# Kernel optimization log

Hardware: AMD Instinct MI355X
Metric: run time of the kernel (lower is better)

The kernel has to match this reference:

```python
import jax, jax.numpy as jnp
import numpy as np

OUT = 7        # RoIPool output_size
STRIDE = 16    # feature map stride (forward does cat_rois[:,1:] *= 1/16)


def setup_inputs() -> dict:
    key = jax.random.key(0)
    k1, k2, k3 = jax.random.split(key, 3)
    B, C, H, W, N = 2, 256, 50, 50, 128
    features = jax.random.normal(k1, (B, C, H, W), jnp.float32)
    im = jax.random.randint(k2, (N,), 0, B).astype(jnp.float32)
    # image-space coords in [0, 16*(H-1)] so rounded feature coords stay in-bounds
    coords = jax.random.uniform(k3, (N, 4), jnp.float32, 0.0, float(STRIDE * (H - 1)))
    x1 = jnp.minimum(coords[:, 0], coords[:, 2])
    x2 = jnp.maximum(coords[:, 0], coords[:, 2])
    y1 = jnp.minimum(coords[:, 1], coords[:, 3])
    y2 = jnp.maximum(coords[:, 1], coords[:, 3])
    cat_rois = jnp.stack([im, x1, y1, x2, y2], axis=1)
    return {"features": features, "cat_rois": cat_rois}


def _roi_pool(features, cat_rois):
    # cat_rois[:,1:] *= 1/16 ; round ; cast to int (as in the torch module)
    rois = cat_rois.at[:, 1:].multiply(1.0 / STRIDE)
    rois = jnp.round(rois).astype(jnp.int32)
    im = rois[:, 0]
    x1, y1, x2, y2 = rois[:, 1], rois[:, 2], rois[:, 3], rois[:, 4]
    h = y2 - y1 + 1  # slice y1:y2+1 -> height
    w = x2 - x1 + 1
    H, W = features.shape[2], features.shape[3]

    i = jnp.arange(OUT)
    # AdaptiveMaxPool2d bin boundaries: start=floor(i*h/OUT), end=ceil((i+1)*h/OUT)
    ys = (i[None, :] * h[:, None]) // OUT + y1[:, None]                 # [N,OUT]
    ye = ((i[None, :] + 1) * h[:, None] + OUT - 1) // OUT + y1[:, None]
    xs = (i[None, :] * w[:, None]) // OUT + x1[:, None]
    xe = ((i[None, :] + 1) * w[:, None] + OUT - 1) // OUT + x1[:, None]

    r = jnp.arange(H)
    c = jnp.arange(W)
    row_mask = (r[None, None, :] >= ys[:, :, None]) & (r[None, None, :] < ye[:, :, None])  # [N,OUT,H]
    col_mask = (c[None, None, :] >= xs[:, :, None]) & (c[None, None, :] < xe[:, :, None])  # [N,OUT,W]

    feat = features[im]  # gather per-roi image: [N,C,H,W]
    neg = jnp.finfo(features.dtype).min
    # row pooling: small fixed loop over OUT bins; select fuses into reduce-max
    rp = jnp.stack(
        [jnp.max(jnp.where(row_mask[:, i, :][:, None, :, None], feat, neg), axis=2)
         for i in range(OUT)], axis=2)  # [N,C,OUT,W]
    out = jnp.stack(
        [jnp.max(jnp.where(col_mask[:, j, :][:, None, None, :], rp, neg), axis=3)
         for j in range(OUT)], axis=3)  # [N,C,OUT,OUT]
    return out


def reference(features, cat_rois):
    return _roi_pool(features, cat_rois)
```

## Files before the change

kernel.cpp:

```cpp
#include <hip/hip_runtime.h>
#include <float.h>

#define OUTP 7
#define NCH 256
#define FH 50
#define FW 50
#define LDS_W 65

__global__ __launch_bounds__(256) void roi_pool_v5(
    const float* __restrict__ features,
    const float* __restrict__ cat_rois,
    float* __restrict__ out)
{
    __shared__ float rowmax[4][OUTP][LDS_W];

    const int lane = threadIdx.x & 63;
    const int quad = threadIdx.x >> 6;
    const int n    = blockIdx.x >> 6;
    const int c    = ((blockIdx.x & 63) << 2) + quad;

    const float* r5 = cat_rois + n * 5;
    const int im = __builtin_amdgcn_readfirstlane((int)rintf(r5[0]));
    const int x1 = __builtin_amdgcn_readfirstlane((int)rintf(r5[1] * 0.0625f));
    const int y1 = __builtin_amdgcn_readfirstlane((int)rintf(r5[2] * 0.0625f));
    const int x2 = __builtin_amdgcn_readfirstlane((int)rintf(r5[3] * 0.0625f));
    const int y2 = __builtin_amdgcn_readfirstlane((int)rintf(r5[4] * 0.0625f));

    const int h = y2 - y1 + 1;
    const int w = x2 - x1 + 1;

    const float* base = features + ((size_t)(im * NCH + c)) * (FH * FW)
                                 + y1 * FW + x1;

    float rm[OUTP];
    #pragma unroll
    for (int i = 0; i < OUTP; ++i) rm[i] = -FLT_MAX;

    if (lane < w) {
        if (h <= 21) {
            #pragma unroll
            for (int i = 0; i < OUTP; ++i) {
                const int ys  = i * h / OUTP;
                const int ye1 = ((i + 1) * h + OUTP - 1) / OUTP - 1;
                float v0 = base[ys * FW + lane];
                float v1 = base[min(ys + 1, ye1) * FW + lane];
                float v2 = base[min(ys + 2, ye1) * FW + lane];
                float v3 = base[min(ys + 3, ye1) * FW + lane];
                rm[i] = fmaxf(fmaxf(v0, v1), fmaxf(v2, v3));
            }
        } else {
            #pragma unroll
            for (int i = 0; i < OUTP; ++i) {
                const int ys  = i * h / OUTP;
                const int ye1 = ((i + 1) * h + OUTP - 1) / OUTP - 1;
                float v[8];
                #pragma unroll
                for (int k = 0; k < 8; ++k)
                    v[k] = base[min(ys + k, ye1) * FW + lane];
                float m01 = fmaxf(v[0], v[1]), m23 = fmaxf(v[2], v[3]);
                float m45 = fmaxf(v[4], v[5]), m67 = fmaxf(v[6], v[7]);
                rm[i] = fmaxf(fmaxf(m01, m23), fmaxf(m45, m67));
            }
        }
    }

    #pragma unroll
    for (int i = 0; i < OUTP; ++i)
        rowmax[quad][i][lane] = rm[i];

    __syncthreads();

    if (lane < OUTP * OUTP) {
        const int i  = lane / OUTP;
        const int j  = lane % OUTP;
        const int xs = j * w / OUTP;
        const int xe = ((j + 1) * w + OUTP - 1) / OUTP;

        float m = -FLT_MAX;
        for (int x = xs; x < xe; ++x)
            m = fmaxf(m, rowmax[quad][i][x]);

        out[(((size_t)n * NCH + c) * OUTP + i) * OUTP + j] = m;
    }
}

extern "C" void kernel_launch(void* const* d_in, const int* in_sizes, int n_in,
                              void* d_out, int out_size, void* d_ws, size_t ws_size,
                              hipStream_t stream) {
    const float* features = (const float*)d_in[0];
    const float* cat_rois = (const float*)d_in[1];
    float* out = (float*)d_out;

    const int N = in_sizes[1] / 5;
    dim3 grid(N * (NCH / 4));
    roi_pool_v5<<<grid, 256, 0, stream>>>(features, cat_rois, out);
}
```

Measured before the change: 73.34 us.

## Pack multiple channels per wavefront by ROI width, 16 channels per block

Each wavefront now handles 4 channels instead of 1. Narrow ROIs (w<=16 or w<=32) pack 4 or 2 channels into the 64 lanes at once so fewer lanes sit idle; wide ROIs loop over the channels. The grid shrinks fourfold and the block-wide __syncthreads is replaced with per-wave LDS waitcnt fences, since each wave only touches its own LDS slice. In exchange there are fewer blocks and more serial work per wave, and correctness now depends on the in-wave LDS ordering being right.

New measurement: 70.80 us. 1.04x faster.

```diff
diff --git a/kernel.cpp b/kernel.cpp
--- a/kernel.cpp
+++ b/kernel.cpp
@@ -5,19 +5,78 @@
 #define NCH 256
 #define FH 50
 #define FW 50
-#define LDS_W 65
+#define LDS_P 65
+#define CH_PER_BLOCK 16
 
-__global__ __launch_bounds__(256) void roi_pool_v5(
+
+template<int KMAX>
+__device__ __forceinline__ void row_phase(const float* __restrict__ lb, int h,
+                                          bool active, float (&rm)[OUTP])
+{
+    #pragma unroll
+    for (int i = 0; i < OUTP; ++i) rm[i] = -FLT_MAX;
+    if (active) {
+        #pragma unroll
+        for (int i = 0; i < OUTP; ++i) {
+            const int ys  = i * h / OUTP;
+            const int ye1 = ((i + 1) * h + OUTP - 1) / OUTP - 1;
+            float v[KMAX];
+            #pragma unroll
+            for (int k = 0; k < KMAX; ++k)
+                v[k] = lb[min(ys + k, ye1) * FW];
+            #pragma unroll
+            for (int s = KMAX / 2; s > 0; s >>= 1)
+                #pragma unroll
+                for (int k = 0; k < s; ++k)
+                    v[k] = fmaxf(v[k], v[k + s]);
+            rm[i] = v[0];
+        }
+    }
+}
+
+template<int SUBW, int NSUB>
+__device__ __forceinline__ void do_rep(const float* __restrict__ lb, bool active,
+                                       int h, int w,
+                                       float (*rowmax)[LDS_P],
+                                       float* __restrict__ outp,
+                                       int lane)
+{
+    float rm[OUTP];
+    if (h <= 21) row_phase<4>(lb, h, active, rm);
+    else         row_phase<8>(lb, h, active, rm);
+
+    asm volatile("s_waitcnt lgkmcnt(0)" ::: "memory");
+    #pragma unroll
+    for (int i = 0; i < OUTP; ++i) rowmax[i][lane] = rm[i];
+    asm volatile("s_waitcnt lgkmcnt(0)" ::: "memory");
+    __builtin_amdgcn_sched_barrier(0);
+
+    if (lane < OUTP * OUTP) {
+        const int i  = lane / OUTP;
+        const int j  = lane - i * OUTP;
+        const int xs = j * w / OUTP;
+        const int xe = ((j + 1) * w + OUTP - 1) / OUTP;
+        #pragma unroll
+        for (int sub = 0; sub < NSUB; ++sub) {
+            float m = -FLT_MAX;
+            for (int x = xs; x < xe; ++x)
+                m = fmaxf(m, rowmax[i][sub * SUBW + x]);
+            outp[sub * (OUTP * OUTP) + lane] = m;
+        }
+    }
+}
+
+__global__ __launch_bounds__(256) void roi_pool_v6(
     const float* __restrict__ features,
     const float* __restrict__ cat_rois,
     float* __restrict__ out)
 {
-    __shared__ float rowmax[4][OUTP][LDS_W];
+    __shared__ float rowmax[4][OUTP][LDS_P];
 
     const int lane = threadIdx.x & 63;
     const int quad = threadIdx.x >> 6;
-    const int n    = blockIdx.x >> 6;
-    const int c    = ((blockIdx.x & 63) << 2) + quad;
+    const int n    = blockIdx.x >> 4;
+    const int c0   = ((blockIdx.x & 15) << 4) + (quad << 2);
 
     const float* r5 = cat_rois + n * 5;
     const int im = __builtin_amdgcn_readfirstlane((int)rintf(r5[0]));
@@ -29,58 +88,28 @@
     const int h = y2 - y1 + 1;
     const int w = x2 - x1 + 1;
 
-    const float* base = features + ((size_t)(im * NCH + c)) * (FH * FW)
-                                 + y1 * FW + x1;
+    const float* base0 = features + ((size_t)(im * NCH + c0)) * (FH * FW)
+                                  + y1 * FW + x1;
+    float* outp = out + ((size_t)n * NCH + c0) * (OUTP * OUTP);
+    float (*rmq)[LDS_P] = rowmax[quad];
 
-    float rm[OUTP];
-    #pragma unroll
-    for (int i = 0; i < OUTP; ++i) rm[i] = -FLT_MAX;
-
-    if (lane < w) {
-        if (h <= 21) {
-            #pragma unroll
-            for (int i = 0; i < OUTP; ++i) {
-                const int ys  = i * h / OUTP;
-                const int ye1 = ((i + 1) * h + OUTP - 1) / OUTP - 1;
-                float v0 = base[ys * FW + lane];
-                float v1 = base[min(ys + 1, ye1) * FW + lane];
-                float v2 = base[min(ys + 2, ye1) * FW + lane];
-                float v3 = base[min(ys + 3, ye1) * FW + lane];
-                rm[i] = fmaxf(fmaxf(v0, v1), fmaxf(v2, v3));
-            }
-        } else {
-            #pragma unroll
-            for (int i = 0; i < OUTP; ++i) {
-                const int ys  = i * h / OUTP;
-                const int ye1 = ((i + 1) * h + OUTP - 1) / OUTP - 1;
-                float v[8];
-                #pragma unroll
-                for (int k = 0; k < 8; ++k)
-                    v[k] = base[min(ys + k, ye1) * FW + lane];
-                float m01 = fmaxf(v[0], v[1]), m23 = fmaxf(v[2], v[3]);
-                float m45 = fmaxf(v[4], v[5]), m67 = fmaxf(v[6], v[7]);
-                rm[i] = fmaxf(fmaxf(m01, m23), fmaxf(m45, m67));
-            }
-        }
-    }
-
-    #pragma unroll
-    for (int i = 0; i < OUTP; ++i)
-        rowmax[quad][i][lane] = rm[i];
-
-    __syncthreads();
-
-    if (lane < OUTP * OUTP) {
-        const int i  = lane / OUTP;
-        const int j  = lane % OUTP;
-        const int xs = j * w / OUTP;
-        const int xe = ((j + 1) * w + OUTP - 1) / OUTP;
-
-        float m = -FLT_MAX;
-        for (int x = xs; x < xe; ++x)
-            m = fmaxf(m, rowmax[quad][i][x]);
-
-        out[(((size_t)n * NCH + c) * OUTP + i) * OUTP + j] = m;
+    if (w <= 16) {
+        const int sub = lane >> 4, col = lane & 15;
+        do_rep<16, 4>(base0 + sub * (FH * FW) + col, col < w, h, w,
+                      rmq, outp, lane);
+    } else if (w <= 32) {
+        const int sub = lane >> 5, col = lane & 31;
+        const bool act = col < w;
+        #pragma unroll
+        for (int rep = 0; rep < 2; ++rep)
+            do_rep<32, 2>(base0 + (2 * rep + sub) * (FH * FW) + col, act, h, w,
+                          rmq, outp + 2 * rep * (OUTP * OUTP), lane);
+    } else {
+        const bool act = lane < w;
+        #pragma unroll
+        for (int rep = 0; rep < 4; ++rep)
+            do_rep<64, 1>(base0 + rep * (FH * FW) + lane, act, h, w,
+                          rmq, outp + rep * (OUTP * OUTP), lane);
     }
 }
 
@@ -92,6 +121,6 @@
     float* out = (float*)d_out;
 
     const int N = in_sizes[1] / 5;
-    dim3 grid(N * (NCH / 4));
-    roi_pool_v5<<<grid, 256, 0, stream>>>(features, cat_rois, out);
+    dim3 grid(N * (NCH / CH_PER_BLOCK));
+    roi_pool_v6<<<grid, 256, 0, stream>>>(features, cat_rois, out);
 }
```
